# Kernel tuning notes

Measured on AMD Instinct MI355X. Metric: run time of the kernel, lower is better.

The kernel has to match this reference:

```python
import jax, jax.numpy as jnp
import numpy as np


def _pad_reflect_br(x):
    # kornia filter2d with a 2x2 kernel pads (0 before, 1 after) in H and W, reflect mode
    return jnp.pad(x, ((0, 1), (0, 1)), mode='reflect')


def _gx(img):
    # correlation with [[-1,1],[-1,1]] at 'same' positions (pad after only)
    p = _pad_reflect_br(img)
    return -p[:-1, :-1] + p[:-1, 1:] - p[1:, :-1] + p[1:, 1:]


def _gy(img):
    # correlation with [[-1,-1],[1,1]]
    p = _pad_reflect_br(img)
    return -p[:-1, :-1] - p[:-1, 1:] + p[1:, :-1] + p[1:, 1:]


def _gsum(img):
    # correlation with all-ones 2x2 kernel
    p = _pad_reflect_br(img)
    return p[:-1, :-1] + p[:-1, 1:] + p[1:, :-1] + p[1:, 1:]


def _box3(x):
    # 3x3 neighborhood sum with zero padding. Zero padding exactly reproduces the
    # truncated patches the python loop sees at the bottom/right borders.
    H, W = x.shape
    p = jnp.pad(x, ((1, 1), (1, 1)))
    out = jnp.zeros_like(x)
    for i in range(3):
        for j in range(3):
            out = out + p[i:i + H, j:j + W]
    return out


def _lk_flow(image_prev, image_next):
    prev = image_prev[0, 0]
    nxt = image_next[0, 0]
    resx = 0.5 * (_gx(prev) + _gx(nxt))
    resy = 0.5 * (_gy(prev) + _gy(nxt))
    resdt = 0.5 * (-_gsum(prev) + _gsum(nxt))

    # structure tensor sums over 3x3 patches (A A^T and b A^T of the original loop)
    Sxx = _box3(resx * resx)
    Syy = _box3(resy * resy)
    Sxy = _box3(resx * resy)
    Sxt = _box3(resdt * resx)
    Syt = _box3(resdt * resy)

    det = Sxx * Syy - Sxy * Sxy
    safe_det = jnp.where(det != 0, det, jnp.ones_like(det))
    u = jnp.where(det != 0, (Syy * Sxt - Sxy * Syt) / safe_det, 0.0)
    v = jnp.where(det != 0, (Sxx * Syt - Sxy * Sxt) / safe_det, 0.0)

    # the python loop starts at i=1, j=1, so row 0 and col 0 stay zero
    u = jnp.pad(u[1:, 1:], ((1, 0), (1, 0)))
    v = jnp.pad(v[1:, 1:], ((1, 0), (1, 0)))
    return jnp.stack([u, v])[None]  # (1, 2, H, W)


def setup_inputs() -> dict:
    key = jax.random.key(0)
    k1, k2 = jax.random.split(key)
    H = W = 2048
    image_prev = jax.random.uniform(k1, (1, 1, H, W), dtype=jnp.float32)
    image_next = jax.random.uniform(k2, (1, 1, H, W), dtype=jnp.float32)
    return {"image_prev": image_prev, "image_next": image_next}


def reference(image_prev, image_next):
    return _lk_flow(image_prev, image_next)
```

## Files before the change

kernel.cpp:

```cpp
#include <hip/hip_runtime.h>


#pragma clang fp contract(off)

#define IMG_H 2048
#define IMG_W 2048
#define TW 32
#define TH 32
#define LDSW 35

__global__ __launch_bounds__(256, 4)
void lk_flow_v7(const float* __restrict__ prev,
                const float* __restrict__ next,
                float* __restrict__ out) {
    #pragma clang fp contract(off)
    __shared__ float srx[(TH + 2) * LDSW];
    __shared__ float sry[(TH + 2) * LDSW];
    __shared__ float srt[(TH + 2) * LDSW];

    const int lin = (int)blockIdx.y * (int)gridDim.x + (int)blockIdx.x;
    const int nl  = (lin >> 3) + (lin & 7) * 512;
    const int r0  = (nl >> 6) * TH;
    const int c0  = (nl & 63) * TW;

    const int tx  = (int)threadIdx.x;
    const int ty  = (int)threadIdx.y;
    const int tid = ty * 8 + tx;

    const bool interior = (r0 > 0) & (r0 + TH + 2 <= IMG_H - 1) &
                          (c0 > 0) & (c0 + TW + 2 <= IMG_W - 1);

    if (interior) {
        #pragma unroll
        for (int pass = 0; pass < 2; ++pass) {
            const int t = tid + pass * 256;
            if (pass == 0 || tid < 16) {
                const int hr = t >> 3;
                const int ch = t & 7;
                const int i0 = (r0 - 1 + hr) * IMG_W + (c0 + ch * 4);
                const int i1 = i0 + IMG_W;
                const float4 P0 = *reinterpret_cast<const float4*>(prev + i0);
                const float4 P1 = *reinterpret_cast<const float4*>(prev + i1);
                const float4 Q0 = *reinterpret_cast<const float4*>(next + i0);
                const float4 Q1 = *reinterpret_cast<const float4*>(next + i1);
                const float p0[5] = {P0.x, P0.y, P0.z, P0.w, prev[i0 + 4]};
                const float p1[5] = {P1.x, P1.y, P1.z, P1.w, prev[i1 + 4]};
                const float q0[5] = {Q0.x, Q0.y, Q0.z, Q0.w, next[i0 + 4]};
                const float q1[5] = {Q1.x, Q1.y, Q1.z, Q1.w, next[i1 + 4]};
                const int base = hr * LDSW + 1 + ch * 4;
                #pragma unroll
                for (int k = 0; k < 4; ++k) {
                    const float Ap = p0[k] + p0[k + 1];
                    const float Aq = q0[k] + q0[k + 1];
                    const float gxp = ((p0[k + 1] - p0[k]) - p1[k]) + p1[k + 1];
                    const float gxq = ((q0[k + 1] - q0[k]) - q1[k]) + q1[k + 1];
                    const float gyp = (p1[k] - Ap) + p1[k + 1];
                    const float gyq = (q1[k] - Aq) + q1[k + 1];
                    const float gsp = (Ap + p1[k]) + p1[k + 1];
                    const float gsq = (Aq + q1[k]) + q1[k + 1];
                    srx[base + k] = 0.5f * (gxp + gxq);
                    sry[base + k] = 0.5f * (gyp + gyq);
                    srt[base + k] = 0.5f * (gsq - gsp);
                }
            }
        }
        if (tid < 68) {
            const int hr = tid >> 1;
            const int e  = tid & 1;
            const int bc = e ? (c0 + TW) : (c0 - 1);
            const int i0 = (r0 - 1 + hr) * IMG_W + bc;
            const int i1 = i0 + IMG_W;
            const float p00 = prev[i0], p01 = prev[i0 + 1];
            const float p10 = prev[i1], p11 = prev[i1 + 1];
            const float q00 = next[i0], q01 = next[i0 + 1];
            const float q10 = next[i1], q11 = next[i1 + 1];
            const float Ap = p00 + p01, Aq = q00 + q01;
            const float gxp = ((p01 - p00) - p10) + p11;
            const float gxq = ((q01 - q00) - q10) + q11;
            const float gyp = (p10 - Ap) + p11;
            const float gyq = (q10 - Aq) + q11;
            const float gsp = (Ap + p10) + p11;
            const float gsq = (Aq + q10) + q11;
            const int o = hr * LDSW + (e ? 33 : 0);
            srx[o] = 0.5f * (gxp + gxq);
            sry[o] = 0.5f * (gyp + gyq);
            srt[o] = 0.5f * (gsq - gsp);
        }
    } else {
        for (int t = tid; t < 34 * 34; t += 256) {
            const int hr = t / 34;
            const int c  = t - hr * 34;
            const int a  = r0 - 1 + hr;
            const int bc = c0 - 1 + c;
            float rx = 0.f, ry = 0.f, rt = 0.f;
            if (a >= 0 && a < IMG_H && bc >= 0 && bc < IMG_W) {
                const int a1 = (a + 1 == IMG_H) ? (IMG_H - 2) : (a + 1);
                const int b1 = (bc + 1 == IMG_W) ? (IMG_W - 2) : (bc + 1);
                const int i0 = a * IMG_W, i1 = a1 * IMG_W;
                const float p00 = prev[i0 + bc], p01 = prev[i0 + b1];
                const float p10 = prev[i1 + bc], p11 = prev[i1 + b1];
                const float q00 = next[i0 + bc], q01 = next[i0 + b1];
                const float q10 = next[i1 + bc], q11 = next[i1 + b1];
                const float Ap = p00 + p01, Aq = q00 + q01;
                const float gxp = ((p01 - p00) - p10) + p11;
                const float gxq = ((q01 - q00) - q10) + q11;
                const float gyp = (p10 - Ap) + p11;
                const float gyq = (q10 - Aq) + q11;
                const float gsp = (Ap + p10) + p11;
                const float gsq = (Aq + q10) + q11;
                rx = 0.5f * (gxp + gxq);
                ry = 0.5f * (gyp + gyq);
                rt = 0.5f * (gsq - gsp);
            }
            const int o = hr * LDSW + c;
            srx[o] = rx; sry[o] = ry; srt[o] = rt;
        }
    }

    __syncthreads();

    const int jb = tx * 4;
    int off = ty * LDSW + jb;

    float aXX[4] = {0.f, 0.f, 0.f, 0.f};
    float aYY[4] = {0.f, 0.f, 0.f, 0.f};
    float aXY[4] = {0.f, 0.f, 0.f, 0.f};
    float aXT[4] = {0.f, 0.f, 0.f, 0.f};
    float aYT[4] = {0.f, 0.f, 0.f, 0.f};

    #pragma unroll
    for (int rr = 0; rr < 3; ++rr) {
        const float* px = srx + off;
        const float* py = sry + off;
        const float* pt = srt + off;
        float X[6], Y[6], T[6];
        #pragma unroll
        for (int k = 0; k < 6; ++k) { X[k] = px[k]; Y[k] = py[k]; T[k] = pt[k]; }
        off += LDSW;
        float xx[6], yy[6], xy[6], xt[6], yt[6];
        #pragma unroll
        for (int k = 0; k < 6; ++k) {
            xx[k] = X[k] * X[k];
            yy[k] = Y[k] * Y[k];
            xy[k] = X[k] * Y[k];
            xt[k] = T[k] * X[k];
            yt[k] = T[k] * Y[k];
        }
        #pragma unroll
        for (int q = 0; q < 4; ++q) {
            aXX[q] += xx[q]; aXX[q] += xx[q + 1]; aXX[q] += xx[q + 2];
            aYY[q] += yy[q]; aYY[q] += yy[q + 1]; aYY[q] += yy[q + 2];
            aXY[q] += xy[q]; aXY[q] += xy[q + 1]; aXY[q] += xy[q + 2];
            aXT[q] += xt[q]; aXT[q] += xt[q + 1]; aXT[q] += xt[q + 2];
            aYT[q] += yt[q]; aYT[q] += yt[q + 1]; aYT[q] += yt[q + 2];
        }
    }

    const int i = r0 + ty;
    float uo[4], vo[4];
    #pragma unroll
    for (int q = 0; q < 4; ++q) {
        const float Sxx = aXX[q], Syy = aYY[q], Sxy = aXY[q];
        const float Sxt = aXT[q], Syt = aYT[q];
        const float t1 = Sxx * Syy;
        const float t2 = Sxy * Sxy;
        const float det = t1 - t2;
        float u = 0.f, v = 0.f;
        if (det != 0.f) {
            const float inv = __builtin_amdgcn_rcpf(det);
            const float n1 = Syy * Sxt - Sxy * Syt;
            const float n2 = Sxx * Syt - Sxy * Sxt;
            u = n1 * inv;
            v = n2 * inv;
        }
        const int j = c0 + jb + q;
        if (i == 0 || j == 0) { u = 0.f; v = 0.f; }
        uo[q] = u; vo[q] = v;
    }
    const int oidx = i * IMG_W + (c0 + jb);
    float4 U = {uo[0], uo[1], uo[2], uo[3]};
    float4 V = {vo[0], vo[1], vo[2], vo[3]};
    *reinterpret_cast<float4*>(out + oidx) = U;
    *reinterpret_cast<float4*>(out + IMG_H * IMG_W + oidx) = V;
}

extern "C" void kernel_launch(void* const* d_in, const int* in_sizes, int n_in,
                              void* d_out, int out_size, void* d_ws, size_t ws_size,
                              hipStream_t stream) {
    const float* prev = (const float*)d_in[0];
    const float* next = (const float*)d_in[1];
    float* out = (float*)d_out;
    dim3 grid(IMG_W / TW, IMG_H / TH);
    dim3 block(8, 32);
    lk_flow_v7<<<grid, block, 0, stream>>>(prev, next, out);
}
```

Measured before the change: 24.38 us.

## Double tile height so each thread computes two output rows with shared row loads

Tile height goes from 32 to 64 rows, and each thread now produces two vertically adjacent outputs. It loads four LDS rows instead of three per output and feeds each row's products into both accumulators. The grid halves, the halo overhead per tile drops, and LDS reads and products per output fall. In exchange the kernel uses more registers (ten accumulator sets), twice the LDS per block, and has fewer blocks in flight, which may reduce occupancy.

```diff
diff --git a/kernel.cpp b/kernel.cpp
--- a/kernel.cpp
+++ b/kernel.cpp
@@ -6,11 +6,11 @@
 #define IMG_H 2048
 #define IMG_W 2048
 #define TW 32
-#define TH 32
+#define TH 64
 #define LDSW 35
 
 __global__ __launch_bounds__(256, 4)
-void lk_flow_v7(const float* __restrict__ prev,
+void lk_flow_v8(const float* __restrict__ prev,
                 const float* __restrict__ next,
                 float* __restrict__ out) {
     #pragma clang fp contract(off)
@@ -19,7 +19,7 @@
     __shared__ float srt[(TH + 2) * LDSW];
 
     const int lin = (int)blockIdx.y * (int)gridDim.x + (int)blockIdx.x;
-    const int nl  = (lin >> 3) + (lin & 7) * 512;
+    const int nl  = (lin >> 3) + (lin & 7) * 256;
     const int r0  = (nl >> 6) * TH;
     const int c0  = (nl & 63) * TW;
 
@@ -32,9 +32,9 @@
 
     if (interior) {
         #pragma unroll
-        for (int pass = 0; pass < 2; ++pass) {
+        for (int pass = 0; pass < 3; ++pass) {
             const int t = tid + pass * 256;
-            if (pass == 0 || tid < 16) {
+            if (pass < 2 || tid < 16) {
                 const int hr = t >> 3;
                 const int ch = t & 7;
                 const int i0 = (r0 - 1 + hr) * IMG_W + (c0 + ch * 4);
@@ -64,7 +64,7 @@
                 }
             }
         }
-        if (tid < 68) {
+        if (tid < (TH + 2) * 2) {
             const int hr = tid >> 1;
             const int e  = tid & 1;
             const int bc = e ? (c0 + TW) : (c0 - 1);
@@ -87,7 +87,7 @@
             srt[o] = 0.5f * (gsq - gsp);
         }
     } else {
-        for (int t = tid; t < 34 * 34; t += 256) {
+        for (int t = tid; t < (TH + 2) * 34; t += 256) {
             const int hr = t / 34;
             const int c  = t - hr * 34;
             const int a  = r0 - 1 + hr;
@@ -120,16 +120,12 @@
     __syncthreads();
 
     const int jb = tx * 4;
-    int off = ty * LDSW + jb;
-
-    float aXX[4] = {0.f, 0.f, 0.f, 0.f};
-    float aYY[4] = {0.f, 0.f, 0.f, 0.f};
-    float aXY[4] = {0.f, 0.f, 0.f, 0.f};
-    float aXT[4] = {0.f, 0.f, 0.f, 0.f};
-    float aYT[4] = {0.f, 0.f, 0.f, 0.f};
+    int off = (ty * 2) * LDSW + jb;
+
+    float aXX[2][4] = {}, aYY[2][4] = {}, aXY[2][4] = {}, aXT[2][4] = {}, aYT[2][4] = {};
 
     #pragma unroll
-    for (int rr = 0; rr < 3; ++rr) {
+    for (int ld = 0; ld < 4; ++ld) {
         const float* px = srx + off;
         const float* py = sry + off;
         const float* pt = srt + off;
@@ -147,41 +143,49 @@
             yt[k] = T[k] * Y[k];
         }
         #pragma unroll
+        for (int o = 0; o < 2; ++o) {
+            if (ld >= o && ld <= o + 2) {
+                #pragma unroll
+                for (int q = 0; q < 4; ++q) {
+                    aXX[o][q] += xx[q]; aXX[o][q] += xx[q + 1]; aXX[o][q] += xx[q + 2];
+                    aYY[o][q] += yy[q]; aYY[o][q] += yy[q + 1]; aYY[o][q] += yy[q + 2];
+                    aXY[o][q] += xy[q]; aXY[o][q] += xy[q + 1]; aXY[o][q] += xy[q + 2];
+                    aXT[o][q] += xt[q]; aXT[o][q] += xt[q + 1]; aXT[o][q] += xt[q + 2];
+                    aYT[o][q] += yt[q]; aYT[o][q] += yt[q + 1]; aYT[o][q] += yt[q + 2];
+                }
+            }
+        }
+    }
+
+    #pragma unroll
+    for (int o = 0; o < 2; ++o) {
+        const int i = r0 + ty * 2 + o;
+        float uo[4], vo[4];
+        #pragma unroll
         for (int q = 0; q < 4; ++q) {
-            aXX[q] += xx[q]; aXX[q] += xx[q + 1]; aXX[q] += xx[q + 2];
-            aYY[q] += yy[q]; aYY[q] += yy[q + 1]; aYY[q] += yy[q + 2];
-            aXY[q] += xy[q]; aXY[q] += xy[q + 1]; aXY[q] += xy[q + 2];
-            aXT[q] += xt[q]; aXT[q] += xt[q + 1]; aXT[q] += xt[q + 2];
-            aYT[q] += yt[q]; aYT[q] += yt[q + 1]; aYT[q] += yt[q + 2];
-        }
+            const float Sxx = aXX[o][q], Syy = aYY[o][q], Sxy = aXY[o][q];
+            const float Sxt = aXT[o][q], Syt = aYT[o][q];
+            const float t1 = Sxx * Syy;
+            const float t2 = Sxy * Sxy;
+            const float det = t1 - t2;
+            float u = 0.f, v = 0.f;
+            if (det != 0.f) {
+                const float inv = __builtin_amdgcn_rcpf(det);
+                const float n1 = Syy * Sxt - Sxy * Syt;
+                const float n2 = Sxx * Syt - Sxy * Sxt;
+                u = n1 * inv;
+                v = n2 * inv;
+            }
+            const int j = c0 + jb + q;
+            if (i == 0 || j == 0) { u = 0.f; v = 0.f; }
+            uo[q] = u; vo[q] = v;
+        }
+        const int oidx = i * IMG_W + (c0 + jb);
+        float4 U = {uo[0], uo[1], uo[2], uo[3]};
+        float4 V = {vo[0], vo[1], vo[2], vo[3]};
+        *reinterpret_cast<float4*>(out + oidx) = U;
+        *reinterpret_cast<float4*>(out + IMG_H * IMG_W + oidx) = V;
     }
-
-    const int i = r0 + ty;
-    float uo[4], vo[4];
-    #pragma unroll
-    for (int q = 0; q < 4; ++q) {
-        const float Sxx = aXX[q], Syy = aYY[q], Sxy = aXY[q];
-        const float Sxt = aXT[q], Syt = aYT[q];
-        const float t1 = Sxx * Syy;
-        const float t2 = Sxy * Sxy;
-        const float det = t1 - t2;
-        float u = 0.f, v = 0.f;
-        if (det != 0.f) {
-            const float inv = __builtin_amdgcn_rcpf(det);
-            const float n1 = Syy * Sxt - Sxy * Syt;
-            const float n2 = Sxx * Syt - Sxy * Sxt;
-            u = n1 * inv;
-            v = n2 * inv;
-        }
-        const int j = c0 + jb + q;
-        if (i == 0 || j == 0) { u = 0.f; v = 0.f; }
-        uo[q] = u; vo[q] = v;
-    }
-    const int oidx = i * IMG_W + (c0 + jb);
-    float4 U = {uo[0], uo[1], uo[2], uo[3]};
-    float4 V = {vo[0], vo[1], vo[2], vo[3]};
-    *reinterpret_cast<float4*>(out + oidx) = U;
-    *reinterpret_cast<float4*>(out + IMG_H * IMG_W + oidx) = V;
 }
 
 extern "C" void kernel_launch(void* const* d_in, const int* in_sizes, int n_in,
@@ -192,5 +196,5 @@
     float* out = (float*)d_out;
     dim3 grid(IMG_W / TW, IMG_H / TH);
     dim3 block(8, 32);
-    lk_flow_v7<<<grid, block, 0, stream>>>(prev, next, out);
+    lk_flow_v8<<<grid, block, 0, stream>>>(prev, next, out);
 }
```

Result: slower. 25.39 us (+4.2%).
